# Kernel optimization log

Hardware: AMD Instinct MI355X
Metric: run time of the kernel (lower is better)

The kernel has to match this reference:

```python
import jax, jax.numpy as jnp
import numpy as np

B, T, S, D = 4, 4, 128, 256  # batch, turns, seq_len, hidden_size
H = D  # GRU units == hidden_size


def setup_inputs() -> dict:
    key = jax.random.key(0)
    ks = jax.random.split(key, 8)
    sc = lambda *sh: float(np.sqrt(2.0 / sum(sh[:2]))) if len(sh) > 1 else 0.05
    return {
        "features": jax.random.normal(ks[0], (B, T, S, D), jnp.float32),
        "w1": jax.random.normal(ks[1], (D, D), jnp.float32) * sc(D, D),
        "w2": jax.random.normal(ks[2], (D, D), jnp.float32) * sc(D, D),
        "bias": jax.random.normal(ks[3], (D,), jnp.float32) * 0.05,
        "v3": jax.random.normal(ks[4], (D,), jnp.float32) * 0.05,
        "gru_kernel": jax.random.normal(ks[5], (2 * D, 3 * H), jnp.float32) * sc(2 * D, 3 * H),
        "gru_rec_kernel": jax.random.normal(ks[6], (H, 3 * H), jnp.float32) * sc(H, 3 * H),
        "gru_bias": jax.random.normal(ks[7], (2, 3 * H), jnp.float32) * 0.05,
    }


def _gru(x, kernel, rec_kernel, bias):
    # x: [N, S, 2D]; Keras GRU (reset_after=True, tanh/sigmoid), h0 = 0.
    b_in, b_rec = bias[0], bias[1]
    xp = x @ kernel + b_in               # [N, S, 3H] input projections
    xp_t = jnp.swapaxes(xp, 0, 1)        # [S, N, 3H]
    h0 = jnp.zeros((x.shape[0], H), x.dtype)

    def step(h, xt):
        rp = h @ rec_kernel + b_rec      # [N, 3H]
        xz, xr, xh = jnp.split(xt, 3, axis=-1)
        rz, rr, rh = jnp.split(rp, 3, axis=-1)
        z = jax.nn.sigmoid(xz + rz)
        r = jax.nn.sigmoid(xr + rr)
        hh = jnp.tanh(xh + r * rh)
        h_new = z * h + (1.0 - z) * hh
        return h_new, h_new

    _, ys = jax.lax.scan(step, h0, xp_t)  # ys: [S, N, H]
    return jnp.swapaxes(ys, 0, 1)         # [N, S, H]


def reference(features, w1, w2, bias, v3, gru_kernel, gru_rec_kernel, gru_bias):
    b, t, s, d = features.shape
    x = features.reshape(b * t, s, d)     # fold turns into batch (same per-utterance math)
    left = jnp.einsum('bsd,dt->bst', x, w1)
    right = jnp.einsum('bsd,dt->bst', x, w2)
    # additive (Bahdanau) scores: [N, s, s, d] intermediate
    temp = jnp.tanh(left[:, :, None, :] + right[:, None, :, :] + bias)
    score = jax.nn.softmax(jnp.einsum('bmnd,d->bmn', temp, v3), axis=-1)
    c = jnp.einsum('bmn,bnd->bmd', score, x)
    p = _gru(jnp.concatenate([x, c], axis=-1), gru_kernel, gru_rec_kernel, gru_bias)
    return p.reshape(b, t, s, H)
```

## Files before the change

### kernel.cpp

```cpp
#include <hip/hip_runtime.h>
#include <hip/hip_bf16.h>

typedef __attribute__((ext_vector_type(8))) short short8;
typedef __attribute__((ext_vector_type(4))) float floatx4;

#define NSEQ 16
#define SEQ 128
#define DIM 256
#define HID 256
#define K3H 768
#define K2D 512
#define LOG2E 1.442695041f
#define LOG2E2 2.885390082f
#define WS_STRIDE 772

__device__ __forceinline__ float frcp(float x) { return __builtin_amdgcn_rcpf(x); }
__device__ __forceinline__ unsigned short bf16bits(float v) {
    unsigned u = __builtin_bit_cast(unsigned, v);
    unsigned r = (u + 0x7FFFu + ((u >> 16) & 1u)) >> 16;
    return (unsigned short)r;
}
__device__ __forceinline__ void load_lds16(const float* gsrc, float* ldsbase) {
    __builtin_amdgcn_global_load_lds(
        (const __attribute__((address_space(1))) void*)gsrc,
        (__attribute__((address_space(3))) void*)ldsbase, 16, 0, 0);
}

__global__ __launch_bounds__(256) void k1_leftright(
        const float* __restrict__ x, const float* __restrict__ w1,
        const float* __restrict__ w2, float* __restrict__ left,
        float* __restrict__ right) {
    __shared__ __align__(16) float xs[8][DIM];
    const int tid = threadIdx.x;
    const int r0 = blockIdx.x * 8;
    #pragma unroll
    for (int i = 0; i < 8; ++i) xs[i][tid] = x[(r0 + i) * DIM + tid];
    __syncthreads();
    float accL[8], accR[8];
    #pragma unroll
    for (int i = 0; i < 8; ++i) { accL[i] = 0.f; accR[i] = 0.f; }
    #pragma unroll 4
    for (int d = 0; d < DIM; ++d) {
        float wa = w1[d * DIM + tid];
        float wb = w2[d * DIM + tid];
        #pragma unroll
        for (int i = 0; i < 8; ++i) {
            float xv = xs[i][d];
            accL[i] = fmaf(xv, wa, accL[i]);
            accR[i] = fmaf(xv, wb, accR[i]);
        }
    }
    #pragma unroll
    for (int i = 0; i < 8; ++i) {
        left[(r0 + i) * DIM + tid]  = accL[i] * LOG2E2;
        right[(r0 + i) * DIM + tid] = accR[i] * LOG2E2;
    }
}

__global__ __launch_bounds__(256) void k2_attn(
        const float* __restrict__ x, const float* __restrict__ left,
        const float* __restrict__ right, const float* __restrict__ bias,
        const float* __restrict__ v3, float* __restrict__ cout) {
    __shared__ __align__(16) float lm[8][DIM];
    __shared__ __align__(16) float v3s[DIM];
    __shared__ __align__(16) float P[8][SEQ];
    const int tid = threadIdx.x;
    const int b  = blockIdx.x >> 4;
    const int m0 = (blockIdx.x & 15) * 8;

    v3s[tid & 255] = v3[tid & 255];
    #pragma unroll
    for (int i = 0; i < 8; ++i)
        lm[i][tid] = left[(size_t)(b * SEQ + m0 + i) * DIM + tid] + bias[tid] * LOG2E2;
    __syncthreads();

    const int mi = tid >> 5;
    const int nl = tid & 31;
    float sacc[4] = {0.f, 0.f, 0.f, 0.f};
    const float4* lv4 = reinterpret_cast<const float4*>(lm[mi]);
    const float4* vv4 = reinterpret_cast<const float4*>(v3s);
    #pragma unroll 2
    for (int d4 = 0; d4 < DIM / 4; ++d4) {
        float4 lv = lv4[d4];
        float4 vv = vv4[d4];
        #pragma unroll
        for (int rep = 0; rep < 4; ++rep) {
            const int n = nl + rep * 32;
            float4 rv = reinterpret_cast<const float4*>(right + (size_t)(b * SEQ + n) * DIM)[d4];
            float t0 = 1.f - 2.f * frcp(1.f + __builtin_amdgcn_exp2f(lv.x + rv.x));
            float t1 = 1.f - 2.f * frcp(1.f + __builtin_amdgcn_exp2f(lv.y + rv.y));
            float t2 = 1.f - 2.f * frcp(1.f + __builtin_amdgcn_exp2f(lv.z + rv.z));
            float t3 = 1.f - 2.f * frcp(1.f + __builtin_amdgcn_exp2f(lv.w + rv.w));
            sacc[rep] = fmaf(t0, vv.x, sacc[rep]);
            sacc[rep] = fmaf(t1, vv.y, sacc[rep]);
            sacc[rep] = fmaf(t2, vv.z, sacc[rep]);
            sacc[rep] = fmaf(t3, vv.w, sacc[rep]);
        }
    }
    #pragma unroll
    for (int rep = 0; rep < 4; ++rep) P[mi][nl + rep * 32] = sacc[rep];
    __syncthreads();

    {
        const int w   = tid >> 6;
        const int lane = tid & 63;
        const int row = w * 2 + (lane >> 5);
        const int g   = lane & 31;
        float v0 = P[row][g], v1 = P[row][g + 32], v2 = P[row][g + 64], v3v = P[row][g + 96];
        float mx = fmaxf(fmaxf(v0, v1), fmaxf(v2, v3v));
        #pragma unroll
        for (int off = 16; off >= 1; off >>= 1) mx = fmaxf(mx, __shfl_xor(mx, off, 64));
        float e0 = __expf(v0 - mx), e1 = __expf(v1 - mx);
        float e2 = __expf(v2 - mx), e3 = __expf(v3v - mx);
        float sm = e0 + e1 + e2 + e3;
        #pragma unroll
        for (int off = 16; off >= 1; off >>= 1) sm += __shfl_xor(sm, off, 64);
        float inv = frcp(sm);
        P[row][g] = e0 * inv; P[row][g + 32] = e1 * inv;
        P[row][g + 64] = e2 * inv; P[row][g + 96] = e3 * inv;
    }
    __syncthreads();

    float acc[8];
    #pragma unroll
    for (int i = 0; i < 8; ++i) acc[i] = 0.f;
    const float* xb = x + (size_t)b * SEQ * DIM;
    for (int nc = 0; nc < SEQ / 4; ++nc) {
        float xv0 = xb[(nc * 4 + 0) * DIM + tid];
        float xv1 = xb[(nc * 4 + 1) * DIM + tid];
        float xv2 = xb[(nc * 4 + 2) * DIM + tid];
        float xv3 = xb[(nc * 4 + 3) * DIM + tid];
        #pragma unroll
        for (int i = 0; i < 8; ++i) {
            float4 pv = *reinterpret_cast<const float4*>(&P[i][nc * 4]);
            acc[i] = fmaf(pv.x, xv0, acc[i]);
            acc[i] = fmaf(pv.y, xv1, acc[i]);
            acc[i] = fmaf(pv.z, xv2, acc[i]);
            acc[i] = fmaf(pv.w, xv3, acc[i]);
        }
    }
    #pragma unroll
    for (int i = 0; i < 8; ++i)
        cout[(size_t)(b * SEQ + m0 + i) * DIM + tid] = acc[i];
}

__global__ __launch_bounds__(512) void k3_mfma(
        const float* __restrict__ x, const float* __restrict__ c,
        const float* __restrict__ gk, const float* __restrict__ gbias,
        float* __restrict__ xp) {
    __shared__ __align__(16) unsigned short As[64][72];
    __shared__ __align__(16) unsigned short Bs[192][72];
    const int tid  = threadIdx.x;
    const int lane = tid & 63;
    const int w    = tid >> 6;
    const int l15  = lane & 15;
    const int g4   = lane >> 4;
    const int wm   = w >> 2;
    const int wn   = w & 3;
    const int m0   = (blockIdx.x & 31) * 64;
    const int n0   = (blockIdx.x >> 5) * 192;

    floatx4 Cf[2][3];
    #pragma unroll
    for (int i = 0; i < 2; ++i)
        #pragma unroll
        for (int j = 0; j < 3; ++j) Cf[i][j] = (floatx4){0.f, 0.f, 0.f, 0.f};

    for (int ch = 0; ch < 8; ++ch) {
        const int kbase = ch * 64;
        #pragma unroll
        for (int q = 0; q < 2; ++q) {
            int fi = q * 512 + tid;
            int row = fi >> 4, kq = (fi & 15) << 2;
            int kg = kbase + kq;
            const float* src = (kg < 256) ? &x[(size_t)(m0 + row) * DIM + kg]
                                          : &c[(size_t)(m0 + row) * DIM + (kg - 256)];
            float4 v = *reinterpret_cast<const float4*>(src);
            unsigned short* dst = &As[row][kq];
            dst[0] = bf16bits(v.x); dst[1] = bf16bits(v.y);
            dst[2] = bf16bits(v.z); dst[3] = bf16bits(v.w);
        }
        #pragma unroll
        for (int q = 0; q < 6; ++q) {
            int fi = q * 512 + tid;
            int krow = fi / 48, nq = (fi % 48) << 2;
            float4 v = *reinterpret_cast<const float4*>(
                &gk[(size_t)(kbase + krow) * K3H + n0 + nq]);
            Bs[nq + 0][krow] = bf16bits(v.x);
            Bs[nq + 1][krow] = bf16bits(v.y);
            Bs[nq + 2][krow] = bf16bits(v.z);
            Bs[nq + 3][krow] = bf16bits(v.w);
        }
        __syncthreads();
        #pragma unroll
        for (int kk = 0; kk < 2; ++kk) {
            short8 af[2], bf[3];
            #pragma unroll
            for (int i = 0; i < 2; ++i)
                af[i] = *reinterpret_cast<const short8*>(&As[wm * 32 + i * 16 + l15][kk * 32 + g4 * 8]);
            #pragma unroll
            for (int j = 0; j < 3; ++j)
                bf[j] = *reinterpret_cast<const short8*>(&Bs[wn * 48 + j * 16 + l15][kk * 32 + g4 * 8]);
            #pragma unroll
            for (int i = 0; i < 2; ++i)
                #pragma unroll
                for (int j = 0; j < 3; ++j)
                    Cf[i][j] = __builtin_amdgcn_mfma_f32_16x16x32_bf16(af[i], bf[j], Cf[i][j], 0, 0, 0);
        }
        __syncthreads();
    }

    #pragma unroll
    for (int j = 0; j < 3; ++j) {
        const int nbase = n0 + wn * 48 + j * 16;
        const int col = nbase + l15;
        const float sc = (nbase >= 512) ? LOG2E2 : LOG2E;
        const float bv = ((col < 512) ? (gbias[col] + gbias[K3H + col]) : gbias[col]) * sc;
        #pragma unroll
        for (int i = 0; i < 2; ++i) {
            const int rbase = m0 + wm * 32 + i * 16 + g4 * 4;
            #pragma unroll
            for (int r = 0; r < 4; ++r)
                xp[(size_t)(rbase + r) * K3H + col] = fmaf(Cf[i][j][r], sc, bv);
        }
    }
}

__global__ __launch_bounds__(512) void k4_gru(
        const float* __restrict__ rec, const float* __restrict__ gbias,
        const float* __restrict__ xp, float* __restrict__ out) {
    __shared__ __align__(16) float ws[16 * WS_STRIDE];
    __shared__ __align__(16) float xq0[K3H], xq1[K3H], xq2[K3H];
    __shared__ __align__(16) unsigned short hbf[2][HID];
    const int tid  = threadIdx.x;
    const int lane = tid & 63;
    const int wv   = tid >> 6;
    const int seq  = blockIdx.x;
    const int l15  = lane & 15;
    const int g4   = lane >> 4;

    short8 Bf[6][8];
    #pragma unroll
    for (int part = 0; part < 16; ++part) {
        #pragma unroll
        for (int q = 0; q < 6; ++q) {
            int fi = q * 512 + tid;
            int row = fi / 192, c4 = fi % 192;
            reinterpret_cast<float4*>(ws)[row * (WS_STRIDE / 4) + c4] =
                reinterpret_cast<const float4*>(rec + part * 16 * K3H)[fi];
        }
        __syncthreads();
        const int kc = part >> 1, half = part & 1;
        #pragma unroll
        for (int u = 0; u < 6; ++u) {
            const float sc = (u >= 4) ? LOG2E2 : LOG2E;
            const int col = (u >> 1) * 256 + (u & 1) * 16 + wv * 32 + l15;
            #pragma unroll
            for (int j = 0; j < 8; ++j) {
                int r = g4 * 8 + j;
                if ((r >> 4) == half)
                    Bf[u][kc][j] = (short)bf16bits(ws[(r & 15) * WS_STRIDE + col] * sc);
            }
        }
        __syncthreads();
    }

    const int dd = wv * 32 + (lane & 31);
    const float brh_l = gbias[K3H + 512 + dd] * LOG2E2;
    const int tsel = (lane >> 4) & 1;

    const float* xps = xp + (size_t)seq * SEQ * K3H;
    float* outs = out + (size_t)seq * SEQ * HID;

    float h = 0.f;
    if (tid < HID) hbf[0][tid] = 0;

    if (wv < 3) {
        load_lds16(xps + wv * 256 + (lane << 2),       xq0 + wv * 256);
        load_lds16(xps + K3H + wv * 256 + (lane << 2), xq1 + wv * 256);
    }
    asm volatile("s_waitcnt vmcnt(0)" ::: "memory");
    __syncthreads();

    float* p0 = xq0;
    float* p1 = xq1;
    float* p2 = xq2;

    #define K4_STEP(s_, CB, NB)                                                         \
    {                                                                                   \
        const int sp = ((s_) + 2 < SEQ) ? (s_) + 2 : SEQ - 1;                           \
        if (wv < 3)                                                                     \
            load_lds16(xps + (size_t)sp * K3H + wv * 256 + (lane << 2), p2 + wv * 256); \
        short8 av[8];                                                                   \
        _Pragma("unroll")                                                               \
        for (int kc = 0; kc < 8; ++kc)                                                  \
            av[kc] = *reinterpret_cast<const short8*>(&hbf[CB][kc * 32 + g4 * 8]);      \
        const float xz = p0[dd];                                                        \
        const float xr = p0[256 + dd];                                                  \
        const float xh = p0[512 + dd];                                                  \
        floatx4 C[6];                                                                   \
        _Pragma("unroll")                                                               \
        for (int u = 0; u < 6; ++u) C[u] = (floatx4){0.f, 0.f, 0.f, 0.f};               \
        _Pragma("unroll")                                                               \
        for (int kc = 0; kc < 8; ++kc) {                                                \
            _Pragma("unroll")                                                           \
            for (int u = 0; u < 6; ++u)                                                 \
                C[u] = __builtin_amdgcn_mfma_f32_16x16x32_bf16(av[kc], Bf[u][kc],       \
                                                               C[u], 0, 0, 0);         \
        }                                                                               \
        if (lane < 32) {                                                                \
            float rz = tsel ? C[1][0] : C[0][0];                                        \
            float rr = tsel ? C[3][0] : C[2][0];                                        \
            float rh = tsel ? C[5][0] : C[4][0];                                        \
            float z  = frcp(1.f + __builtin_amdgcn_exp2f(-(rz + xz)));                  \
            float r  = frcp(1.f + __builtin_amdgcn_exp2f(-(rr + xr)));                  \
            float th = fmaf(r, rh + brh_l, xh);                                         \
            float hh = 1.f - 2.f * frcp(1.f + __builtin_amdgcn_exp2f(th));              \
            h = hh + z * (h - hh);                                                      \
            hbf[NB][dd] = bf16bits(h);                                                  \
            outs[(s_) * HID + dd] = h;                                                  \
        }                                                                               \
        asm volatile("s_waitcnt vmcnt(3) lgkmcnt(0)\n\ts_barrier" ::: "memory");        \
        float* tmp_ = p0; p0 = p1; p1 = p2; p2 = tmp_;                                  \
    }

    for (int s = 0; s < SEQ; s += 2) {
        K4_STEP(s,     0, 1)
        K4_STEP(s + 1, 1, 0)
    }
    #undef K4_STEP
}

extern "C" void kernel_launch(void* const* d_in, const int* in_sizes, int n_in,
                              void* d_out, int out_size, void* d_ws, size_t ws_size,
                              hipStream_t stream) {
    const float* feat = (const float*)d_in[0];
    const float* w1   = (const float*)d_in[1];
    const float* w2   = (const float*)d_in[2];
    const float* bias = (const float*)d_in[3];
    const float* v3   = (const float*)d_in[4];
    const float* gk   = (const float*)d_in[5];
    const float* grk  = (const float*)d_in[6];
    const float* gb   = (const float*)d_in[7];
    float* out = (float*)d_out;

    char* wsb = (char*)d_ws;
    float* left  = (float*)(wsb);
    float* right = (float*)(wsb + (size_t)2 * 1024 * 1024);
    float* cbuf  = (float*)(wsb + (size_t)4 * 1024 * 1024);
    float* xp    = (float*)(wsb + (size_t)6 * 1024 * 1024);

    k1_leftright<<<2048 / 8, 256, 0, stream>>>(feat, w1, w2, left, right);
    k2_attn<<<NSEQ * 16, 256, 0, stream>>>(feat, left, right, bias, v3, cbuf);
    k3_mfma<<<128, 512, 0, stream>>>(feat, cbuf, gk, gb, xp);
    k4_gru<<<NSEQ, 512, 0, stream>>>(grk, gb, xp, out);
}
```

Baseline: 239.6 us.

## Compute left/right projections with bf16 MFMA tiles instead of scalar FMA

Replaces the scalar-FMA projection kernel with a tiled bf16 MFMA GEMM. Each block computes a 64x256 tile of either left or right from inputs converted to bf16 in LDS. This cuts the ALU-bound fp32 matmul time. In exchange it uses only 64 blocks and lowers the precision of the attention logits to bf16.

Measured after the change: 244.1 us. No clear change (+1.9%).

```diff
diff --git a/kernel.cpp b/kernel.cpp
--- a/kernel.cpp
+++ b/kernel.cpp
@@ -26,34 +26,74 @@
         (__attribute__((address_space(3))) void*)ldsbase, 16, 0, 0);
 }
 
-__global__ __launch_bounds__(256) void k1_leftright(
+__global__ __launch_bounds__(512) void k1_mfma(
         const float* __restrict__ x, const float* __restrict__ w1,
         const float* __restrict__ w2, float* __restrict__ left,
         float* __restrict__ right) {
-    __shared__ __align__(16) float xs[8][DIM];
-    const int tid = threadIdx.x;
-    const int r0 = blockIdx.x * 8;
-    #pragma unroll
-    for (int i = 0; i < 8; ++i) xs[i][tid] = x[(r0 + i) * DIM + tid];
-    __syncthreads();
-    float accL[8], accR[8];
-    #pragma unroll
-    for (int i = 0; i < 8; ++i) { accL[i] = 0.f; accR[i] = 0.f; }
-    #pragma unroll 4
-    for (int d = 0; d < DIM; ++d) {
-        float wa = w1[d * DIM + tid];
-        float wb = w2[d * DIM + tid];
-        #pragma unroll
-        for (int i = 0; i < 8; ++i) {
-            float xv = xs[i][d];
-            accL[i] = fmaf(xv, wa, accL[i]);
-            accR[i] = fmaf(xv, wb, accR[i]);
-        }
-    }
-    #pragma unroll
-    for (int i = 0; i < 8; ++i) {
-        left[(r0 + i) * DIM + tid]  = accL[i] * LOG2E2;
-        right[(r0 + i) * DIM + tid] = accR[i] * LOG2E2;
+    __shared__ __align__(16) unsigned short As[64][40];
+    __shared__ __align__(16) unsigned short Bs[256][40];
+    const int tid  = threadIdx.x;
+    const int lane = tid & 63;
+    const int w    = tid >> 6;
+    const int l15  = lane & 15;
+    const int g4   = lane >> 4;
+    const int wm   = w >> 2;
+    const int wn   = w & 3;
+    const int m0   = (blockIdx.x >> 1) * 64;
+    const float* B = (blockIdx.x & 1) ? w2 : w1;
+    float* outp    = (blockIdx.x & 1) ? right : left;
+
+    floatx4 Cf[2][4];
+    #pragma unroll
+    for (int i = 0; i < 2; ++i)
+        #pragma unroll
+        for (int j = 0; j < 4; ++j) Cf[i][j] = (floatx4){0.f, 0.f, 0.f, 0.f};
+
+    for (int ch = 0; ch < 8; ++ch) {
+        const int kbase = ch * 32;
+        {
+            int row = tid >> 3, kq = (tid & 7) << 2;
+            float4 v = *reinterpret_cast<const float4*>(&x[(size_t)(m0 + row) * DIM + kbase + kq]);
+            unsigned short* dst = &As[row][kq];
+            dst[0] = bf16bits(v.x); dst[1] = bf16bits(v.y);
+            dst[2] = bf16bits(v.z); dst[3] = bf16bits(v.w);
+        }
+        #pragma unroll
+        for (int q = 0; q < 4; ++q) {
+            int fi = q * 512 + tid;
+            int krow = fi >> 6, nq = (fi & 63) << 2;
+            float4 v = *reinterpret_cast<const float4*>(&B[(size_t)(kbase + krow) * DIM + nq]);
+            Bs[nq + 0][krow] = bf16bits(v.x);
+            Bs[nq + 1][krow] = bf16bits(v.y);
+            Bs[nq + 2][krow] = bf16bits(v.z);
+            Bs[nq + 3][krow] = bf16bits(v.w);
+        }
+        __syncthreads();
+        short8 af[2], bf[4];
+        #pragma unroll
+        for (int i = 0; i < 2; ++i)
+            af[i] = *reinterpret_cast<const short8*>(&As[wm * 32 + i * 16 + l15][g4 * 8]);
+        #pragma unroll
+        for (int j = 0; j < 4; ++j)
+            bf[j] = *reinterpret_cast<const short8*>(&Bs[wn * 64 + j * 16 + l15][g4 * 8]);
+        #pragma unroll
+        for (int i = 0; i < 2; ++i)
+            #pragma unroll
+            for (int j = 0; j < 4; ++j)
+                Cf[i][j] = __builtin_amdgcn_mfma_f32_16x16x32_bf16(af[i], bf[j], Cf[i][j], 0, 0, 0);
+        __syncthreads();
+    }
+
+    #pragma unroll
+    for (int j = 0; j < 4; ++j) {
+        const int col = wn * 64 + j * 16 + l15;
+        #pragma unroll
+        for (int i = 0; i < 2; ++i) {
+            const int rbase = m0 + wm * 32 + i * 16 + g4 * 4;
+            #pragma unroll
+            for (int r = 0; r < 4; ++r)
+                outp[(size_t)(rbase + r) * DIM + col] = Cf[i][j][r] * LOG2E2;
+        }
     }
 }
 
@@ -350,7 +390,7 @@
     float* cbuf  = (float*)(wsb + (size_t)4 * 1024 * 1024);
     float* xp    = (float*)(wsb + (size_t)6 * 1024 * 1024);
 
-    k1_leftright<<<2048 / 8, 256, 0, stream>>>(feat, w1, w2, left, right);
+    k1_mfma<<<64, 512, 0, stream>>>(feat, w1, w2, left, right);
     k2_attn<<<NSEQ * 16, 256, 0, stream>>>(feat, left, right, bias, v3, cbuf);
     k3_mfma<<<128, 512, 0, stream>>>(feat, cbuf, gk, gb, xp);
     k4_gru<<<NSEQ, 512, 0, stream>>>(grk, gb, xp, out);
```
